# Performance work log

Hardware: AMD Instinct MI355X
Metric: run time of the kernel (lower is better)

Reference implementation:

```python
import jax, jax.numpy as jnp
import numpy as np

D_MODEL = 1024
N_HEADS = 16
D_K = D_MODEL // N_HEADS


def setup_inputs() -> dict:
    key = jax.random.key(0)
    ks = jax.random.split(key, 9)
    s = 1.0 / np.sqrt(D_MODEL)
    return {
        "x": jax.random.normal(ks[0], (4, 2048, D_MODEL), dtype=jnp.float32),
        "Wq": jax.random.normal(ks[1], (D_MODEL, D_MODEL), dtype=jnp.float32) * s,
        "bq": jax.random.normal(ks[2], (D_MODEL,), dtype=jnp.float32) * 0.01,
        "Wk": jax.random.normal(ks[3], (D_MODEL, D_MODEL), dtype=jnp.float32) * s,
        "bk": jax.random.normal(ks[4], (D_MODEL,), dtype=jnp.float32) * 0.01,
        "Wv": jax.random.normal(ks[5], (D_MODEL, D_MODEL), dtype=jnp.float32) * s,
        "bv": jax.random.normal(ks[6], (D_MODEL,), dtype=jnp.float32) * 0.01,
        "Wo": jax.random.normal(ks[7], (D_MODEL, D_MODEL), dtype=jnp.float32) * s,
        "bo": jax.random.normal(ks[8], (D_MODEL,), dtype=jnp.float32) * 0.01,
    }


def reference(x, Wq, bq, Wk, bk, Wv, bv, Wo, bo):
    B, S, _ = x.shape
    # projections (torch Linear: x @ W.T + b; here W stored as [in, out])
    q = (x @ Wq + bq).reshape(B, S, N_HEADS, D_K).transpose(0, 2, 1, 3)  # [B,H,S,Dk]
    k = (x @ Wk + bk).reshape(B, S, N_HEADS, D_K).transpose(0, 2, 1, 3)
    v = (x @ Wv + bv).reshape(B, S, N_HEADS, D_K).transpose(0, 2, 1, 3)
    scale = 1.0 / np.sqrt(D_K).astype(np.float32)
    scores = jnp.einsum("bhsd,bhtd->bhst", q, k) * scale  # [B,H,S,S]
    attn = jax.nn.softmax(scores, axis=-1)
    ctx = jnp.einsum("bhst,bhtd->bhsd", attn, v)  # [B,H,S,Dk]
    ctx = ctx.transpose(0, 2, 1, 3).reshape(B, S, D_MODEL)
    return ctx @ Wo + bo
```

## Files before the change

### kernel.cpp

```cpp
#include <hip/hip_runtime.h>
#include <math.h>

#define DMODEL 1024
#define NHEADS 16
#define DKDIM  64
#define SEQLEN 2048
#define NBATCH 4
#define MTOT   (NBATCH * SEQLEN)

typedef __attribute__((ext_vector_type(8)))  short short8;
typedef __attribute__((ext_vector_type(4)))  float f32x4;
typedef __attribute__((ext_vector_type(16))) float f32x16;

__device__ __forceinline__ unsigned short f2bf(float x) {
    unsigned u = __builtin_bit_cast(unsigned, x);
    unsigned r = (u + 0x7fffu + ((u >> 16) & 1u)) >> 16;
    return (unsigned short)r;
}

__device__ __forceinline__ void gload16(const void* g, void* l) {
    __builtin_amdgcn_global_load_lds(
        (const __attribute__((address_space(1))) void*)g,
        (__attribute__((address_space(3))) void*)l, 16, 0, 0);
}

__global__ __launch_bounds__(256)
void convert_x_kernel(const float* __restrict__ x, unsigned short* __restrict__ xb)
{
    const size_t i = ((size_t)blockIdx.x * 256 + threadIdx.x) * 8;
    const float4 a = *(const float4*)&x[i];
    const float4 b = *(const float4*)&x[i + 4];
    union { unsigned short u[8]; uint4 q; } p;
    p.u[0] = f2bf(a.x); p.u[1] = f2bf(a.y); p.u[2] = f2bf(a.z); p.u[3] = f2bf(a.w);
    p.u[4] = f2bf(b.x); p.u[5] = f2bf(b.y); p.u[6] = f2bf(b.z); p.u[7] = f2bf(b.w);
    *(uint4*)&xb[i] = p.q;
}

__global__ __launch_bounds__(256)
void convert_w_kernel(const float* __restrict__ W0, const float* __restrict__ W1,
                      const float* __restrict__ W2, const float* __restrict__ W3,
                      unsigned short* __restrict__ wt)
{
    const int z = blockIdx.z;
    const float* W = (z == 0) ? W0 : (z == 1) ? W1 : (z == 2) ? W2 : W3;
    unsigned short* dst = wt + (size_t)z * DMODEL * DMODEL;
    const int n0 = blockIdx.x * 64, k0 = blockIdx.y * 64;
    __shared__ float T[64][65];
    const int t = threadIdx.x;
    const int r0 = t >> 4, c0 = (t & 15) << 2;
#pragma unroll
    for (int u = 0; u < 4; ++u) {
        const float4 wv = *(const float4*)&W[(size_t)(k0 + r0 + u * 16) * DMODEL + n0 + c0];
        T[c0 + 0][r0 + u * 16] = wv.x;
        T[c0 + 1][r0 + u * 16] = wv.y;
        T[c0 + 2][r0 + u * 16] = wv.z;
        T[c0 + 3][r0 + u * 16] = wv.w;
    }
    __syncthreads();
    const int rn = t >> 2, ck = (t & 3) << 4;
    union { unsigned short u16[16]; uint4 q[2]; } pk;
#pragma unroll
    for (int e = 0; e < 16; ++e) pk.u16[e] = f2bf(T[rn][ck + e]);
    *(uint4*)&dst[(size_t)(n0 + rn) * DMODEL + k0 + ck]     = pk.q[0];
    *(uint4*)&dst[(size_t)(n0 + rn) * DMODEL + k0 + ck + 8] = pk.q[1];
}

template<int OMODE>
__device__ __forceinline__
void gemm_core(const unsigned short* __restrict__ A, const unsigned short* __restrict__ Bt,
               const float* __restrict__ bias, void* __restrict__ outv, const float scl)
{
    __shared__ __align__(16) char As[128 * 128];
    __shared__ __align__(16) char Bs[128 * 128];

    const int t  = threadIdx.x;
    const int l  = t & 63, w = t >> 6;
    const int g  = (l >> 4), lr = l & 15;
    const int wr = w >> 1, wc = w & 1;
    const int swz = (lr & 7) << 4;

    const int flat = (blockIdx.y << 3) | blockIdx.x;
    const int sid  = ((flat & 7) << 6) | (flat >> 3);
    const int m0 = (sid >> 3) << 7;
    const int n0 = (sid & 7) << 7;

    f32x4 acc[4][4];
#pragma unroll
    for (int i = 0; i < 4; ++i)
#pragma unroll
        for (int j = 0; j < 4; ++j) acc[i][j] = (f32x4){0.f, 0.f, 0.f, 0.f};

    for (int k0 = 0; k0 < DMODEL; k0 += 64) {
        __syncthreads();
#pragma unroll
        for (int qd = 0; qd < 4; ++qd) {
            const int o   = (t + qd * 256) << 4;
            const int row = o >> 7;
            const int c   = (o & 127) ^ ((row & 7) << 4);
            gload16((const char*)A  + (((size_t)(m0 + row) * DMODEL + k0) << 1) + c, As + o);
            gload16((const char*)Bt + (((size_t)(n0 + row) * DMODEL + k0) << 1) + c, Bs + o);
        }
        __syncthreads();

        short8 af[4][2], bf[4][2];
#pragma unroll
        for (int i = 0; i < 4; ++i)
#pragma unroll
            for (int kk = 0; kk < 2; ++kk) {
                const int off = (kk * 64 + g * 16) ^ swz;
                af[i][kk] = *(const short8*)(As + (wr * 64 + i * 16 + lr) * 128 + off);
                bf[i][kk] = *(const short8*)(Bs + (wc * 64 + i * 16 + lr) * 128 + off);
            }
        __builtin_amdgcn_s_setprio(1);
#pragma unroll
        for (int kk = 0; kk < 2; ++kk)
#pragma unroll
            for (int i = 0; i < 4; ++i)
#pragma unroll
                for (int j = 0; j < 4; ++j)
                    acc[i][j] = __builtin_amdgcn_mfma_f32_16x16x32_bf16(
                        af[i][kk], bf[j][kk], acc[i][j], 0, 0, 0);
        __builtin_amdgcn_s_setprio(0);
    }

    float bj[4];
#pragma unroll
    for (int j = 0; j < 4; ++j) bj[j] = bias[n0 + wc * 64 + j * 16 + lr];

#pragma unroll
    for (int i = 0; i < 4; ++i)
#pragma unroll
        for (int j = 0; j < 4; ++j) {
            const int mb = m0 + wr * 64 + i * 16 + g * 4;
            const int n  = n0 + wc * 64 + j * 16 + lr;
            float v[4];
#pragma unroll
            for (int r = 0; r < 4; ++r) v[r] = (acc[i][j][r] + bj[j]) * scl;
            if (OMODE == 0) {
                unsigned short* outp = (unsigned short*)outv;
#pragma unroll
                for (int r = 0; r < 4; ++r)
                    outp[(size_t)(mb + r) * DMODEL + n] = f2bf(v[r]);
            } else if (OMODE == 1) {
                unsigned short* outp = (unsigned short*)outv;
                const int b = mb >> 11, s = mb & (SEQLEN - 1);
                const size_t idx = (((size_t)(b * NHEADS + (n >> 6)) * DKDIM + (n & 63)) << 11) + s;
                uint2 pk;
                pk.x = (unsigned)f2bf(v[0]) | ((unsigned)f2bf(v[1]) << 16);
                pk.y = (unsigned)f2bf(v[2]) | ((unsigned)f2bf(v[3]) << 16);
                *(uint2*)&outp[idx] = pk;
            } else {
                float* outp = (float*)outv;
#pragma unroll
                for (int r = 0; r < 4; ++r)
                    outp[(size_t)(mb + r) * DMODEL + n] = v[r];
            }
        }
}

#define QSCALE 0.1803368801111137f

__global__ __launch_bounds__(256)
void qkv_gemm_kernel(const unsigned short* __restrict__ xb, const unsigned short* __restrict__ wt,
                     const float* __restrict__ bq, const float* __restrict__ bk,
                     const float* __restrict__ bv,
                     unsigned short* __restrict__ Qb, unsigned short* __restrict__ Kb,
                     unsigned short* __restrict__ Vt)
{
    if (blockIdx.z == 0)      gemm_core<0>(xb, wt,                      bq, Qb, QSCALE);
    else if (blockIdx.z == 1) gemm_core<0>(xb, wt + DMODEL * DMODEL,     bk, Kb, 1.0f);
    else                      gemm_core<1>(xb, wt + 2 * DMODEL * DMODEL, bv, Vt, 1.0f);
}

__global__ __launch_bounds__(256)
void out_gemm_kernel(const unsigned short* __restrict__ ctx, const unsigned short* __restrict__ wt,
                     const float* __restrict__ bo, float* __restrict__ out)
{
    gemm_core<2>(ctx, wt + 3 * DMODEL * DMODEL, bo, out, 1.0f);
}

__device__ __forceinline__
void attn_body(const char* __restrict__ Kbuf, const char* __restrict__ Vbuf,
               const short8 (&qf)[4], f32x16 (&po)[2], float& lsum_part,
               int q32, int hi, int swz)
{
    f32x16 sc[2];
#pragma unroll
    for (int r = 0; r < 16; ++r) { sc[0][r] = 0.f; sc[1][r] = 0.f; }
#pragma unroll
    for (int i = 0; i < 2; ++i) {
        short8 kf[4];
#pragma unroll
        for (int kk = 0; kk < 4; ++kk)
            kf[kk] = *(const short8*)(Kbuf + (i * 32 + q32) * 128 + ((kk * 32 + hi * 16) ^ swz));
        __builtin_amdgcn_s_setprio(1);
#pragma unroll
        for (int kk = 0; kk < 4; ++kk)
            sc[i] = __builtin_amdgcn_mfma_f32_32x32x16_bf16(kf[kk], qf[kk], sc[i], 0, 0, 0);
        __builtin_amdgcn_s_setprio(0);
    }

    float a0 = 0.f, a1 = 0.f, a2 = 0.f, a3 = 0.f;
#pragma unroll
    for (int i = 0; i < 2; ++i)
#pragma unroll
        for (int r = 0; r < 16; r += 4) {
            const float p0 = exp2f(sc[i][r + 0]);
            const float p1 = exp2f(sc[i][r + 1]);
            const float p2 = exp2f(sc[i][r + 2]);
            const float p3 = exp2f(sc[i][r + 3]);
            sc[i][r + 0] = p0; sc[i][r + 1] = p1;
            sc[i][r + 2] = p2; sc[i][r + 3] = p3;
            a0 += p0; a1 += p1; a2 += p2; a3 += p3;
        }
    lsum_part += (a0 + a1) + (a2 + a3);

    short8 pf[4];
#pragma unroll
    for (int ks = 0; ks < 4; ++ks) {
        const f32x16& st = sc[ks >> 1];
        const int bse = (ks & 1) * 8;
        unsigned wA0, wA1, wB0, wB1;
        asm("v_cvt_pk_bf16_f32 %0, %1, %2" : "=v"(wA0) : "v"(st[bse + 0]), "v"(st[bse + 1]));
        asm("v_cvt_pk_bf16_f32 %0, %1, %2" : "=v"(wA1) : "v"(st[bse + 2]), "v"(st[bse + 3]));
        asm("v_cvt_pk_bf16_f32 %0, %1, %2" : "=v"(wB0) : "v"(st[bse + 4]), "v"(st[bse + 5]));
        asm("v_cvt_pk_bf16_f32 %0, %1, %2" : "=v"(wB1) : "v"(st[bse + 6]), "v"(st[bse + 7]));
        asm volatile("v_permlane32_swap_b32 %0, %1" : "+v"(wA0), "+v"(wB0));
        asm volatile("v_permlane32_swap_b32 %0, %1" : "+v"(wA1), "+v"(wB1));
        union { unsigned u[4]; short8 s; } pk;
        pk.u[0] = wA0; pk.u[1] = wA1; pk.u[2] = wB0; pk.u[3] = wB1;
        pf[ks] = pk.s;
    }

#pragma unroll
    for (int i = 0; i < 2; ++i) {
        short8 vf[4];
#pragma unroll
        for (int ks = 0; ks < 4; ++ks)
            vf[ks] = *(const short8*)(Vbuf + (i * 32 + q32) * 128 + ((ks * 32 + hi * 16) ^ swz));
        __builtin_amdgcn_s_setprio(1);
#pragma unroll
        for (int ks = 0; ks < 4; ++ks)
            po[i] = __builtin_amdgcn_mfma_f32_32x32x16_bf16(vf[ks], pf[ks], po[i], 0, 0, 0);
        __builtin_amdgcn_s_setprio(0);
    }
}

__global__ __launch_bounds__(512)
void attn_kernel(const unsigned short* __restrict__ Qb, const unsigned short* __restrict__ Kb,
                 const unsigned short* __restrict__ Vt, unsigned short* __restrict__ ctx)
{
    __shared__ __align__(16) char smem[49152];

    const int t   = threadIdx.x;
    const int l   = t & 63, w = t >> 6;
    const int q32 = l & 31, hi = l >> 5;
    const int swz = (q32 & 7) << 4;

    const int flat = (blockIdx.y << 3) | blockIdx.x;
    const int sid  = ((flat & 7) << 6) | (flat >> 3);
    const int qt = sid & 7;
    const int bh = sid >> 3;
    const int b  = bh >> 4, h = bh & 15;
    const int coln = h * DKDIM;

    const size_t qrow  = (size_t)b * SEQLEN + qt * 256 + w * 32 + q32;
    const size_t krow0 = (size_t)b * SEQLEN;
    const size_t vbase = (size_t)(b * NHEADS + h) * DKDIM * SEQLEN;

    short8 qf[4];
#pragma unroll
    for (int kk = 0; kk < 4; ++kk)
        qf[kk] = *(const short8*)(Qb + qrow * DMODEL + coln + kk * 16 + hi * 8);

    f32x16 po[2];
#pragma unroll
    for (int r = 0; r < 16; ++r) { po[0][r] = 0.f; po[1][r] = 0.f; }
    float lsum_part = 0.f;

    const int so   = t << 4;
    const int srow = so >> 7;
    const int sc_  = (so & 127) ^ ((srow & 7) << 4);

#define STAGE(bufidx, kt)                                                                    \
    do {                                                                                     \
        gload16((const char*)Kb + (((krow0 + (kt) * 64 + srow) * DMODEL + coln) << 1) + sc_, \
                smem + (bufidx) * 8192 + so);                                                \
        gload16((const char*)Vt + ((vbase + (size_t)srow * SEQLEN + (kt) * 64) << 1) + sc_,  \
                smem + 24576 + (bufidx) * 8192 + so);                                        \
    } while (0)

    STAGE(0, 0);
    STAGE(1, 1);

#pragma unroll 1
    for (int kt = 0; kt < 31; ++kt) {
        asm volatile("s_waitcnt vmcnt(2)" ::: "memory");
        __builtin_amdgcn_s_barrier();
        if (kt + 2 < 32) STAGE((kt + 2) % 3, kt + 2);
        const int buf = kt % 3;
        attn_body(smem + buf * 8192, smem + 24576 + buf * 8192,
                  qf, po, lsum_part, q32, hi, swz);
    }
    asm volatile("s_waitcnt vmcnt(0)" ::: "memory");
    __builtin_amdgcn_s_barrier();
    attn_body(smem + 8192, smem + 24576 + 8192, qf, po, lsum_part, q32, hi, swz);

    __syncthreads();

    const float lsum = lsum_part + __shfl_xor(lsum_part, 32);
    const float inv  = 1.0f / lsum;
    char* T = smem + w * 4096;
#pragma unroll
    for (int i = 0; i < 2; ++i)
#pragma unroll
        for (int g4 = 0; g4 < 4; ++g4) {
            const int d0 = i * 32 + g4 * 8 + hi * 4;
            uint2 pk;
            pk.x = (unsigned)f2bf(po[i][g4 * 4 + 0] * inv) | ((unsigned)f2bf(po[i][g4 * 4 + 1] * inv) << 16);
            pk.y = (unsigned)f2bf(po[i][g4 * 4 + 2] * inv) | ((unsigned)f2bf(po[i][g4 * 4 + 3] * inv) << 16);
            *(uint2*)(T + ((q32 * 128 + d0 * 2) ^ swz)) = pk;
        }
    __syncthreads();
#pragma unroll
    for (int pass = 0; pass < 4; ++pass) {
        const int o   = (l + pass * 64) << 4;
        const int row = o >> 7;
        const int c   = o & 127;
        const uint4 val = *(const uint4*)(T + (o ^ ((row & 7) << 4)));
        const size_t token = (size_t)b * SEQLEN + qt * 256 + w * 32 + row;
        *(uint4*)&ctx[token * DMODEL + coln + (c >> 1)] = val;
    }
#undef STAGE
}

extern "C" void kernel_launch(void* const* d_in, const int* in_sizes, int n_in,
                              void* d_out, int out_size, void* d_ws, size_t ws_size,
                              hipStream_t stream)
{
    const float* x  = (const float*)d_in[0];
    const float* Wq = (const float*)d_in[1];
    const float* bq = (const float*)d_in[2];
    const float* Wk = (const float*)d_in[3];
    const float* bk = (const float*)d_in[4];
    const float* Wv = (const float*)d_in[5];
    const float* bv = (const float*)d_in[6];
    const float* Wo = (const float*)d_in[7];
    const float* bo = (const float*)d_in[8];
    float* out = (float*)d_out;

    const size_t NE = (size_t)MTOT * DMODEL;
    unsigned short* xb  = (unsigned short*)d_ws;
    unsigned short* wt  = xb  + NE;
    unsigned short* Qb  = wt  + (size_t)4 * DMODEL * DMODEL;
    unsigned short* Kb  = Qb  + NE;
    unsigned short* Vt  = Kb  + NE;
    unsigned short* ctx = Vt  + NE;

    convert_x_kernel<<<dim3(NE / (256 * 8)), 256, 0, stream>>>(x, xb);
    convert_w_kernel<<<dim3(16, 16, 4), 256, 0, stream>>>(Wq, Wk, Wv, Wo, wt);
    qkv_gemm_kernel<<<dim3(8, 64, 3), 256, 0, stream>>>(xb, wt, bq, bk, bv, Qb, Kb, Vt);
    attn_kernel<<<dim3(SEQLEN / 256, NBATCH * NHEADS), dim3(512), 0, stream>>>(Qb, Kb, Vt, ctx);
    out_gemm_kernel<<<dim3(8, 64), 256, 0, stream>>>(ctx, wt, bo, out);
}
```

Before: 193.4 us.

## Compute softmax row sums via MFMA with ones and interleave QK/PV per half

Replaces the per-lane VALU summation of exponentials and the final cross-half shuffle with an extra MFMA against a ones vector, so the row-sum comes out of the matrix unit using the same bf16-rounded probabilities. The attention body is also restructured to process the 64-key tile in two halves, doing QK, exp2 (now the raw hardware intrinsic), conversion and PV per half, which lowers live score registers and interleaves compute. The cost is 2 extra MFMAs per half and a 16-register accumulator for the sums.

```diff
diff --git a/kernel.cpp b/kernel.cpp
--- a/kernel.cpp
+++ b/kernel.cpp
@@ -181,67 +181,58 @@
 
 __device__ __forceinline__
 void attn_body(const char* __restrict__ Kbuf, const char* __restrict__ Vbuf,
-               const short8 (&qf)[4], f32x16 (&po)[2], float& lsum_part,
+               const short8 (&qf)[4], const short8 ones,
+               f32x16 (&po)[2], f32x16& po_l,
                int q32, int hi, int swz)
 {
-    f32x16 sc[2];
-#pragma unroll
-    for (int r = 0; r < 16; ++r) { sc[0][r] = 0.f; sc[1][r] = 0.f; }
-#pragma unroll
-    for (int i = 0; i < 2; ++i) {
+#pragma unroll
+    for (int hf = 0; hf < 2; ++hf) {
+        f32x16 s;
+#pragma unroll
+        for (int r = 0; r < 16; ++r) s[r] = 0.f;
         short8 kf[4];
 #pragma unroll
         for (int kk = 0; kk < 4; ++kk)
-            kf[kk] = *(const short8*)(Kbuf + (i * 32 + q32) * 128 + ((kk * 32 + hi * 16) ^ swz));
+            kf[kk] = *(const short8*)(Kbuf + (hf * 32 + q32) * 128 + ((kk * 32 + hi * 16) ^ swz));
         __builtin_amdgcn_s_setprio(1);
 #pragma unroll
         for (int kk = 0; kk < 4; ++kk)
-            sc[i] = __builtin_amdgcn_mfma_f32_32x32x16_bf16(kf[kk], qf[kk], sc[i], 0, 0, 0);
+            s = __builtin_amdgcn_mfma_f32_32x32x16_bf16(kf[kk], qf[kk], s, 0, 0, 0);
         __builtin_amdgcn_s_setprio(0);
-    }
-
-    float a0 = 0.f, a1 = 0.f, a2 = 0.f, a3 = 0.f;
-#pragma unroll
-    for (int i = 0; i < 2; ++i)
-#pragma unroll
-        for (int r = 0; r < 16; r += 4) {
-            const float p0 = exp2f(sc[i][r + 0]);
-            const float p1 = exp2f(sc[i][r + 1]);
-            const float p2 = exp2f(sc[i][r + 2]);
-            const float p3 = exp2f(sc[i][r + 3]);
-            sc[i][r + 0] = p0; sc[i][r + 1] = p1;
-            sc[i][r + 2] = p2; sc[i][r + 3] = p3;
-            a0 += p0; a1 += p1; a2 += p2; a3 += p3;
-        }
-    lsum_part += (a0 + a1) + (a2 + a3);
-
-    short8 pf[4];
-#pragma unroll
-    for (int ks = 0; ks < 4; ++ks) {
-        const f32x16& st = sc[ks >> 1];
-        const int bse = (ks & 1) * 8;
-        unsigned wA0, wA1, wB0, wB1;
-        asm("v_cvt_pk_bf16_f32 %0, %1, %2" : "=v"(wA0) : "v"(st[bse + 0]), "v"(st[bse + 1]));
-        asm("v_cvt_pk_bf16_f32 %0, %1, %2" : "=v"(wA1) : "v"(st[bse + 2]), "v"(st[bse + 3]));
-        asm("v_cvt_pk_bf16_f32 %0, %1, %2" : "=v"(wB0) : "v"(st[bse + 4]), "v"(st[bse + 5]));
-        asm("v_cvt_pk_bf16_f32 %0, %1, %2" : "=v"(wB1) : "v"(st[bse + 6]), "v"(st[bse + 7]));
-        asm volatile("v_permlane32_swap_b32 %0, %1" : "+v"(wA0), "+v"(wB0));
-        asm volatile("v_permlane32_swap_b32 %0, %1" : "+v"(wA1), "+v"(wB1));
-        union { unsigned u[4]; short8 s; } pk;
-        pk.u[0] = wA0; pk.u[1] = wA1; pk.u[2] = wB0; pk.u[3] = wB1;
-        pf[ks] = pk.s;
-    }
-
-#pragma unroll
-    for (int i = 0; i < 2; ++i) {
-        short8 vf[4];
-#pragma unroll
-        for (int ks = 0; ks < 4; ++ks)
-            vf[ks] = *(const short8*)(Vbuf + (i * 32 + q32) * 128 + ((ks * 32 + hi * 16) ^ swz));
+
+#pragma unroll
+        for (int r = 0; r < 16; ++r) s[r] = __builtin_amdgcn_exp2f(s[r]);
+
+        short8 pf[2];
+#pragma unroll
+        for (int j = 0; j < 2; ++j) {
+            const int bse = j * 8;
+            unsigned wA0, wA1, wB0, wB1;
+            asm("v_cvt_pk_bf16_f32 %0, %1, %2" : "=v"(wA0) : "v"(s[bse + 0]), "v"(s[bse + 1]));
+            asm("v_cvt_pk_bf16_f32 %0, %1, %2" : "=v"(wA1) : "v"(s[bse + 2]), "v"(s[bse + 3]));
+            asm("v_cvt_pk_bf16_f32 %0, %1, %2" : "=v"(wB0) : "v"(s[bse + 4]), "v"(s[bse + 5]));
+            asm("v_cvt_pk_bf16_f32 %0, %1, %2" : "=v"(wB1) : "v"(s[bse + 6]), "v"(s[bse + 7]));
+            asm volatile("v_permlane32_swap_b32 %0, %1" : "+v"(wA0), "+v"(wB0));
+            asm volatile("v_permlane32_swap_b32 %0, %1" : "+v"(wA1), "+v"(wB1));
+            union { unsigned u[4]; short8 s8; } pk;
+            pk.u[0] = wA0; pk.u[1] = wA1; pk.u[2] = wB0; pk.u[3] = wB1;
+            pf[j] = pk.s8;
+        }
+
+        short8 vf0[2], vf1[2];
+#pragma unroll
+        for (int j = 0; j < 2; ++j) {
+            const int ks = hf * 2 + j;
+            vf0[j] = *(const short8*)(Vbuf + q32 * 128 + ((ks * 32 + hi * 16) ^ swz));
+            vf1[j] = *(const short8*)(Vbuf + (32 + q32) * 128 + ((ks * 32 + hi * 16) ^ swz));
+        }
         __builtin_amdgcn_s_setprio(1);
 #pragma unroll
-        for (int ks = 0; ks < 4; ++ks)
-            po[i] = __builtin_amdgcn_mfma_f32_32x32x16_bf16(vf[ks], pf[ks], po[i], 0, 0, 0);
+        for (int j = 0; j < 2; ++j) {
+            po[0] = __builtin_amdgcn_mfma_f32_32x32x16_bf16(vf0[j], pf[j], po[0], 0, 0, 0);
+            po[1] = __builtin_amdgcn_mfma_f32_32x32x16_bf16(vf1[j], pf[j], po[1], 0, 0, 0);
+            po_l  = __builtin_amdgcn_mfma_f32_32x32x16_bf16(ones,   pf[j], po_l,  0, 0, 0);
+        }
         __builtin_amdgcn_s_setprio(0);
     }
 }
@@ -273,10 +264,13 @@
     for (int kk = 0; kk < 4; ++kk)
         qf[kk] = *(const short8*)(Qb + qrow * DMODEL + coln + kk * 16 + hi * 8);
 
-    f32x16 po[2];
-#pragma unroll
-    for (int r = 0; r < 16; ++r) { po[0][r] = 0.f; po[1][r] = 0.f; }
-    float lsum_part = 0.f;
+    short8 ones;
+#pragma unroll
+    for (int e = 0; e < 8; ++e) ones[e] = (short)0x3F80;
+
+    f32x16 po[2], po_l;
+#pragma unroll
+    for (int r = 0; r < 16; ++r) { po[0][r] = 0.f; po[1][r] = 0.f; po_l[r] = 0.f; }
 
     const int so   = t << 4;
     const int srow = so >> 7;
@@ -300,16 +294,15 @@
         if (kt + 2 < 32) STAGE((kt + 2) % 3, kt + 2);
         const int buf = kt % 3;
         attn_body(smem + buf * 8192, smem + 24576 + buf * 8192,
-                  qf, po, lsum_part, q32, hi, swz);
+                  qf, ones, po, po_l, q32, hi, swz);
     }
     asm volatile("s_waitcnt vmcnt(0)" ::: "memory");
     __builtin_amdgcn_s_barrier();
-    attn_body(smem + 8192, smem + 24576 + 8192, qf, po, lsum_part, q32, hi, swz);
+    attn_body(smem + 8192, smem + 24576 + 8192, qf, ones, po, po_l, q32, hi, swz);
 
     __syncthreads();
 
-    const float lsum = lsum_part + __shfl_xor(lsum_part, 32);
-    const float inv  = 1.0f / lsum;
+    const float inv = 1.0f / po_l[0];
     char* T = smem + w * 4096;
 #pragma unroll
     for (int i = 0; i < 2; ++i)
```

Result: faster. 178.6 us (-7.6%).
